# Kernel optimization log

Measured on AMD Instinct MI355X. Metric: run time of the kernel, lower is better.

The kernel has to match this reference:

```python
import jax, jax.numpy as jnp
import numpy as np


def _aggregate(x, w, k, pad):
    """Involution-style per-pixel local conv.
    x: [N, C, H, W]; w: [N, heads, wc, k*k, H, W] (stride=1, dilation=1, zero pad).
    Returns [N, heads, C, H, W].
    """
    N, C, H, W = x.shape
    heads, wc = w.shape[1], w.shape[2]
    G = C // wc  # channel groups sharing the same per-pixel weights (c % wc)
    xp = jnp.pad(x, ((0, 0), (0, 0), (pad, pad), (pad, pad)))
    # unfold: [N, C, k*k, H, W] via k*k static shifted slices (no dynamic indexing)
    patches = jnp.stack(
        [xp[:, :, i:i + H, j:j + W] for i in range(k) for j in range(k)], axis=2
    )
    p = patches.reshape(N, G, wc, k * k, H, W)
    # out[n, e, g, v, h, w] = sum_k w[n, e, v, k, h, w] * p[n, g, v, k, h, w]
    out = jnp.einsum('nevkhw,ngvkhw->negvhw', w, p)
    return out.reshape(N, heads, C, H, W)


def reference(x, weight1, weight2):
    out1 = _aggregate(x, weight1, 3, 1)  # 3x3 branch, pad=1
    out2 = _aggregate(x, weight2, 5, 2)  # 5x5 branch, pad=2
    # output layout [N, 2, heads, C, H, W] matching the CUDA index arithmetic
    return jnp.stack([out1, out2], axis=1)


def setup_inputs() -> dict:
    key = jax.random.key(0)
    k1, k2, k3 = jax.random.split(key, 3)
    N, C, H, W = 4, 256, 56, 56
    heads, wc = 1, 32
    x = jax.random.normal(k1, (N, C, H, W), dtype=jnp.float32)
    weight1 = jax.random.normal(k2, (N, heads, wc, 9, H, W), dtype=jnp.float32)
    weight2 = jax.random.normal(k3, (N, heads, wc, 25, H, W), dtype=jnp.float32)
    return {"x": x, "weight1": weight1, "weight2": weight2}
```

## Files before the change

### kernel.cpp

```cpp
#include <hip/hip_runtime.h>


#define N_  4
#define C_  256
#define H_  56
#define W_  56
#define HW_ 3136
#define WC_ 32

#define TILE    14
#define LROWS   18
#define LSTRIDE 64

__global__ __launch_bounds__(256) void lconv_kernel(
    const float* __restrict__ x,
    const float* __restrict__ w1,
    const float* __restrict__ w2,
    float* __restrict__ out)
{
    __shared__ float lds[4 * LROWS * LSTRIDE];

    const int b    = blockIdx.x;
    const int tile = b & 3;
    const int gsel = (b >> 2) & 1;
    const int v    = (b >> 3) & 31;
    const int n    = b >> 8;
    const int r0   = tile * TILE;
    const int nv   = n * WC_ + v;
    const int tid  = threadIdx.x;

    for (int idx = tid; idx < 4 * LROWS * 14; idx += 256) {
        const int c4 = idx % 14;
        const int t2 = idx / 14;
        const int lr = t2 % LROWS;
        const int pl = t2 / LROWS;
        const int gr = r0 - 2 + lr;
        float4 val = make_float4(0.f, 0.f, 0.f, 0.f);
        if (gr >= 0 && gr < H_) {
            const int ch = gsel * 128 + pl * 32 + v;
            val = *(const float4*)(x + (size_t)(n * C_ + ch) * HW_ + gr * W_ + c4 * 4);
        }
        float* lp = &lds[(pl * LROWS + lr) * LSTRIDE + 4 * c4 + 2];
        *(float2*)(lp)     = make_float2(val.x, val.y);
        *(float2*)(lp + 2) = make_float2(val.z, val.w);
    }
    for (int idx = tid; idx < 4 * LROWS * 4; idx += 256) {
        const int k  = idx & 3;
        const int t2 = idx >> 2;
        const int lr = t2 % LROWS;
        const int pl = t2 / LROWS;
        const int slot = (k < 2) ? k : (56 + k);
        lds[(pl * LROWS + lr) * LSTRIDE + slot] = 0.f;
    }
    __syncthreads();

    if (tid >= TILE * 14) return;

    const int row = tid / 14;
    const int s   = tid % 14;
    const int wb  = 4 * s;
    const int h   = r0 + row;
    const int hw  = h * W_ + wb;

    const float* w1t = w1 + (size_t)nv * 9  * HW_ + hw;
    const float* w2t = w2 + (size_t)nv * 25 * HW_ + hw;

    float a1[4][4], a2[4][4];
    #pragma unroll
    for (int g = 0; g < 4; ++g)
        #pragma unroll
        for (int p = 0; p < 4; ++p) { a1[g][p] = 0.f; a2[g][p] = 0.f; }

    #pragma unroll 1
    for (int di = 0; di < 5; ++di) {
        const bool inner = (di >= 1) && (di <= 3);

        float wr2[5][4];
        #pragma unroll
        for (int dj = 0; dj < 5; ++dj) {
            const float4 t = *(const float4*)(w2t + (size_t)(di * 5 + dj) * HW_);
            wr2[dj][0] = t.x; wr2[dj][1] = t.y; wr2[dj][2] = t.z; wr2[dj][3] = t.w;
        }
        float wr1[3][4];
        #pragma unroll
        for (int dj = 0; dj < 3; ++dj)
            #pragma unroll
            for (int p = 0; p < 4; ++p) wr1[dj][p] = 0.f;
        if (inner) {
            #pragma unroll
            for (int dj = 0; dj < 3; ++dj) {
                const float4 t = *(const float4*)(w1t + (size_t)((di - 1) * 3 + dj) * HW_);
                wr1[dj][0] = t.x; wr1[dj][1] = t.y; wr1[dj][2] = t.z; wr1[dj][3] = t.w;
            }
        }

        #pragma unroll
        for (int g = 0; g < 4; ++g) {
            const float* lp = &lds[(g * LROWS + row + di) * LSTRIDE + wb];
            const float4 xa = *(const float4*)(lp);
            const float4 xb4 = *(const float4*)(lp + 4);
            const float xw[8] = {xa.x, xa.y, xa.z, xa.w, xb4.x, xb4.y, xb4.z, xb4.w};

            #pragma unroll
            for (int dj = 0; dj < 5; ++dj)
                #pragma unroll
                for (int p = 0; p < 4; ++p)
                    a2[g][p] += wr2[dj][p] * xw[p + dj];
            if (inner) {
                #pragma unroll
                for (int dj = 0; dj < 3; ++dj)
                    #pragma unroll
                    for (int p = 0; p < 4; ++p)
                        a1[g][p] += wr1[dj][p] * xw[p + dj + 1];
            }
        }
    }

    const int c0 = gsel * 128 + v;
    float* o1 = out + ((size_t)(n * 2 + 0) * C_ + c0) * HW_ + hw;
    float* o2 = out + ((size_t)(n * 2 + 1) * C_ + c0) * HW_ + hw;
    #pragma unroll
    for (int g = 0; g < 4; ++g) {
        *(float4*)(o1 + (size_t)g * WC_ * HW_) =
            make_float4(a1[g][0], a1[g][1], a1[g][2], a1[g][3]);
        *(float4*)(o2 + (size_t)g * WC_ * HW_) =
            make_float4(a2[g][0], a2[g][1], a2[g][2], a2[g][3]);
    }
}

extern "C" void kernel_launch(void* const* d_in, const int* in_sizes, int n_in,
                              void* d_out, int out_size, void* d_ws, size_t ws_size,
                              hipStream_t stream) {
    const float* x  = (const float*)d_in[0];
    const float* w1 = (const float*)d_in[1];
    const float* w2 = (const float*)d_in[2];
    float* out = (float*)d_out;

    dim3 grid(4 * 2 * 32 * 4), block(256);
    hipLaunchKernelGGL(lconv_kernel, grid, block, 0, stream, x, w1, w2, out);
}
```

Baseline: 114.2 us.

## Prefetch weights before LDS fill, double-buffer 5x5 rows, split branches

```diff
diff --git a/kernel.cpp b/kernel.cpp
--- a/kernel.cpp
+++ b/kernel.cpp
@@ -20,14 +20,35 @@
 {
     __shared__ float lds[4 * LROWS * LSTRIDE];
 
-    const int b    = blockIdx.x;
-    const int tile = b & 3;
-    const int gsel = (b >> 2) & 1;
-    const int v    = (b >> 3) & 31;
-    const int n    = b >> 8;
-    const int r0   = tile * TILE;
-    const int nv   = n * WC_ + v;
-    const int tid  = threadIdx.x;
+    const int b     = blockIdx.x;
+    const int tile  = b & 3;
+    const int vlow  = (b >> 2) & 1;
+    const int gsel  = (b >> 3) & 1;
+    const int vhigh = (b >> 4) & 15;
+    const int n     = b >> 8;
+    const int v     = (vhigh << 1) | vlow;
+    const int r0    = tile * TILE;
+    const int nv    = n * WC_ + v;
+    const int tid   = threadIdx.x;
+
+    const int row = tid / 14;
+    const int s   = tid - row * 14;
+    const int wb  = 4 * s;
+    const int h   = r0 + row;
+    const int hc  = (h < H_) ? h : (H_ - 1);
+    const int hw  = hc * W_ + wb;
+
+    const float* w1t = w1 + (size_t)nv * 9  * HW_ + hw;
+    const float* w2t = w2 + (size_t)nv * 25 * HW_ + hw;
+
+    float4 w2cur[5], w2nxt[5];
+    #pragma unroll
+    for (int dj = 0; dj < 5; ++dj)
+        w2cur[dj] = *(const float4*)(w2t + (size_t)dj * HW_);
+    float4 w1all[9];
+    #pragma unroll
+    for (int p = 0; p < 9; ++p)
+        w1all[p] = *(const float4*)(w1t + (size_t)p * HW_);
 
     for (int idx = tid; idx < 4 * LROWS * 14; idx += 256) {
         const int c4 = idx % 14;
@@ -56,76 +77,76 @@
 
     if (tid >= TILE * 14) return;
 
-    const int row = tid / 14;
-    const int s   = tid % 14;
-    const int wb  = 4 * s;
-    const int h   = r0 + row;
-    const int hw  = h * W_ + wb;
+    const int c0 = gsel * 128 + v;
 
-    const float* w1t = w1 + (size_t)nv * 9  * HW_ + hw;
-    const float* w2t = w2 + (size_t)nv * 25 * HW_ + hw;
-
-    float a1[4][4], a2[4][4];
+    float a2[4][4];
     #pragma unroll
     for (int g = 0; g < 4; ++g)
         #pragma unroll
-        for (int p = 0; p < 4; ++p) { a1[g][p] = 0.f; a2[g][p] = 0.f; }
+        for (int p = 0; p < 4; ++p) a2[g][p] = 0.f;
 
     #pragma unroll 1
     for (int di = 0; di < 5; ++di) {
-        const bool inner = (di >= 1) && (di <= 3);
-
-        float wr2[5][4];
-        #pragma unroll
-        for (int dj = 0; dj < 5; ++dj) {
-            const float4 t = *(const float4*)(w2t + (size_t)(di * 5 + dj) * HW_);
-            wr2[dj][0] = t.x; wr2[dj][1] = t.y; wr2[dj][2] = t.z; wr2[dj][3] = t.w;
+        if (di < 4) {
+            #pragma unroll
+            for (int dj = 0; dj < 5; ++dj)
+                w2nxt[dj] = *(const float4*)(w2t + (size_t)((di + 1) * 5 + dj) * HW_);
         }
-        float wr1[3][4];
-        #pragma unroll
-        for (int dj = 0; dj < 3; ++dj)
-            #pragma unroll
-            for (int p = 0; p < 4; ++p) wr1[dj][p] = 0.f;
-        if (inner) {
-            #pragma unroll
-            for (int dj = 0; dj < 3; ++dj) {
-                const float4 t = *(const float4*)(w1t + (size_t)((di - 1) * 3 + dj) * HW_);
-                wr1[dj][0] = t.x; wr1[dj][1] = t.y; wr1[dj][2] = t.z; wr1[dj][3] = t.w;
-            }
-        }
-
         #pragma unroll
         for (int g = 0; g < 4; ++g) {
             const float* lp = &lds[(g * LROWS + row + di) * LSTRIDE + wb];
-            const float4 xa = *(const float4*)(lp);
+            const float4 xa  = *(const float4*)(lp);
             const float4 xb4 = *(const float4*)(lp + 4);
             const float xw[8] = {xa.x, xa.y, xa.z, xa.w, xb4.x, xb4.y, xb4.z, xb4.w};
-
             #pragma unroll
-            for (int dj = 0; dj < 5; ++dj)
+            for (int dj = 0; dj < 5; ++dj) {
+                const float* wr = (const float*)&w2cur[dj];
                 #pragma unroll
                 for (int p = 0; p < 4; ++p)
-                    a2[g][p] += wr2[dj][p] * xw[p + dj];
-            if (inner) {
+                    a2[g][p] += wr[p] * xw[p + dj];
+            }
+        }
+        if (di < 4) {
+            #pragma unroll
+            for (int dj = 0; dj < 5; ++dj) w2cur[dj] = w2nxt[dj];
+        }
+    }
+
+    float* o2 = out + ((size_t)(n * 2 + 1) * C_ + c0) * HW_ + hw;
+    #pragma unroll
+    for (int g = 0; g < 4; ++g)
+        *(float4*)(o2 + (size_t)g * WC_ * HW_) =
+            make_float4(a2[g][0], a2[g][1], a2[g][2], a2[g][3]);
+
+    float a1[4][4];
+    #pragma unroll
+    for (int g = 0; g < 4; ++g)
+        #pragma unroll
+        for (int p = 0; p < 4; ++p) a1[g][p] = 0.f;
+
+    #pragma unroll 1
+    for (int di = 0; di < 3; ++di) {
+        #pragma unroll
+        for (int g = 0; g < 4; ++g) {
+            const float* lp = &lds[(g * LROWS + row + 1 + di) * LSTRIDE + wb];
+            const float4 xa  = *(const float4*)(lp);
+            const float4 xb4 = *(const float4*)(lp + 4);
+            const float xw[8] = {xa.x, xa.y, xa.z, xa.w, xb4.x, xb4.y, xb4.z, xb4.w};
+            #pragma unroll
+            for (int dj = 0; dj < 3; ++dj) {
+                const float* wr = (const float*)&w1all[di * 3 + dj];
                 #pragma unroll
-                for (int dj = 0; dj < 3; ++dj)
-                    #pragma unroll
-                    for (int p = 0; p < 4; ++p)
-                        a1[g][p] += wr1[dj][p] * xw[p + dj + 1];
+                for (int p = 0; p < 4; ++p)
+                    a1[g][p] += wr[p] * xw[p + dj + 1];
             }
         }
     }
 
-    const int c0 = gsel * 128 + v;
     float* o1 = out + ((size_t)(n * 2 + 0) * C_ + c0) * HW_ + hw;
-    float* o2 = out + ((size_t)(n * 2 + 1) * C_ + c0) * HW_ + hw;
     #pragma unroll
-    for (int g = 0; g < 4; ++g) {
+    for (int g = 0; g < 4; ++g)
         *(float4*)(o1 + (size_t)g * WC_ * HW_) =
             make_float4(a1[g][0], a1[g][1], a1[g][2], a1[g][3]);
-        *(float4*)(o2 + (size_t)g * WC_ * HW_) =
-            make_float4(a2[g][0], a2[g][1], a2[g][2], a2[g][3]);
-    }
 }
 
 extern "C" void kernel_launch(void* const* d_in, const int* in_sizes, int n_in,
@@ -136,6 +157,6 @@
     const float* w2 = (const float*)d_in[2];
     float* out = (float*)d_out;
 
-    dim3 grid(4 * 2 * 32 * 4), block(256);
+    dim3 grid(1024), block(256);
     hipLaunchKernelGGL(lconv_kernel, grid, block, 0, stream, x, w1, w2, out);
 }
```

Result: slower. 126.7 us (+10.9%).
